# Kernel optimization log

Measured on AMD Instinct MI355X. Metric: run time of the kernel, lower is better.

## Reference

```python
import jax, jax.numpy as jnp
import numpy as np

EPS = 1e-12  # F.normalize default eps

def _l2norm(x, axis):
    n = jnp.sqrt(jnp.sum(x * x, axis=axis, keepdims=True))
    return x / jnp.maximum(n, EPS)

def setup_inputs() -> dict:
    key = jax.random.key(0)
    ks = jax.random.split(key, 12)
    N, D, L, H, R = 65536, 384, 64, 64, 8
    return {
        "enhanced_posts_embeddings": jax.random.normal(ks[0], (N, D), jnp.float32),
        "selected_reasoning_embeddings": jax.random.normal(ks[1], (N, D), jnp.float32),
        "llm_embeddings": jax.random.normal(ks[2], (L, D), jnp.float32),
        "random_num": jax.random.uniform(ks[3], (N, 1), jnp.float32),
        # gate: Linear(2D -> R)
        "gate_w": jax.random.normal(ks[4], (2 * D, R), jnp.float32) * 0.02,
        "gate_b": jnp.zeros((R,), jnp.float32),
        # per-router U: Linear(2D -> H), V: Linear(D -> H)
        "U_w": jax.random.normal(ks[5], (R, 2 * D, H), jnp.float32) * 0.02,
        "U_b": jnp.zeros((R, H), jnp.float32),
        "V_w": jax.random.normal(ks[6], (R, D, H), jnp.float32) * 0.02,
        "V_b": jnp.zeros((R, H), jnp.float32),
    }

def reference(enhanced_posts_embeddings, selected_reasoning_embeddings,
              llm_embeddings, random_num,
              gate_w, gate_b, U_w, U_b, V_w, V_b):
    K = 2
    R = gate_b.shape[0]
    AUX_COEF = 0.05
    TEMP = 1.0

    x = jnp.concatenate([enhanced_posts_embeddings,
                         selected_reasoning_embeddings], axis=-1)  # [N, 2D]
    logits = x @ gate_w + gate_b                                   # [N, R]
    probs = jax.nn.softmax(logits, axis=-1)
    topk_vals, topk_idxs = jax.lax.top_k(logits, K)                # [N, K]
    topk_mask = jax.nn.one_hot(topk_idxs, R, dtype=jnp.float32).sum(axis=1)  # [N, R]

    aux_loss = R * (probs.mean(axis=0) * topk_mask.mean(axis=0)).sum() * AUX_COEF

    # All-router projections (dense over routers), then gather the top-k.
    Ux = _l2norm(jnp.einsum('nd,rdh->nrh', x, U_w) + U_b, axis=-1)            # [N, R, H]
    Vl = _l2norm(jnp.einsum('ld,rdh->rlh', llm_embeddings, V_w) + V_b[:, None, :], axis=-1)  # [R, L, H]
    scores_all = jax.nn.softmax(jnp.einsum('nrh,rlh->nrl', Ux, Vl) / TEMP, axis=-1)  # [N, R, L]

    router_outputs = jnp.take_along_axis(scores_all, topk_idxs[:, :, None], axis=1)  # [N, K, L]
    gate_weights = jax.nn.softmax(topk_vals, axis=-1)[:, :, None]                    # [N, K, 1]
    llm_probs = jnp.sum(router_outputs * gate_weights, axis=1)                       # [N, L]

    scores_cumsum = jnp.cumsum(llm_probs, axis=1)
    selected_index = jnp.argmax((scores_cumsum > random_num).astype(jnp.float32), axis=1)  # [N]
    log_probs = jnp.log(jnp.take_along_axis(llm_probs, selected_index[:, None], axis=1))   # [N, 1]
    return selected_index, log_probs, aux_loss
```

## Files before the change

### kernel.cpp

```cpp
#include <hip/hip_runtime.h>
#include <math.h>

#define AUX_SLOTS 1024
#define CAP 24576

__global__ __launch_bounds__(256) void gate_vl_kernel(
    const float* __restrict__ llm, const float* __restrict__ Vw,
    const float* __restrict__ Vb, float* __restrict__ vl,
    const float* __restrict__ eh, const float* __restrict__ sr,
    const float* __restrict__ gw, const float* __restrict__ gb,
    int* __restrict__ ent, float* __restrict__ ewt,
    float* __restrict__ aux, int* __restrict__ cnt, int N)
{
    __shared__ float red[256];
    __shared__ int lcnt[8], lbase[8], lcur[8];
    __shared__ int   s_r01[32];
    __shared__ float s_w0[32], s_w1[32];
    int tid = threadIdx.x;

    if (blockIdx.x < 512) {
        int b = blockIdx.x;
        int r = b >> 6, l = b & 63;
        int t = tid & 63, q = tid >> 6;
        const float* w  = Vw + ((size_t)r * 384 + q * 96) * 64 + t;
        const float* xr = llm + l * 384 + q * 96;
        float acc = 0.f;
#pragma unroll 4
        for (int d = 0; d < 96; ++d) acc += xr[d] * w[(size_t)d * 64];
        red[tid] = acc;
        __syncthreads();
        if (q == 0) {
            acc = red[t] + red[64 + t] + red[128 + t] + red[192 + t] + Vb[r * 64 + t];
            float ss = acc * acc;
#pragma unroll
            for (int m = 1; m < 64; m <<= 1) ss += __shfl_xor(ss, m);
            float inv = 1.0f / fmaxf(sqrtf(ss), 1e-12f);
            vl[((size_t)r * 64 + t) * 64 + l] = acc * inv;
        }
        return;
    }

    int bx = blockIdx.x - 512;
    if (tid < 8) { lcnt[tid] = 0; lcur[tid] = 0; }
    __syncthreads();
    int wave = tid >> 6, lane = tid & 63;
    int wgid = bx * 4 + wave;
    float gbr[8];
#pragma unroll
    for (int r = 0; r < 8; ++r) gbr[r] = gb[r];
    float aux_acc = 0.f;

    for (int rr = 0; rr < 8; ++rr) {
        int row = wgid * 8 + rr;
        const float4* pa = (const float4*)(eh + (size_t)row * 384);
        const float4* pb = (const float4*)(sr + (size_t)row * 384);
        float4 xv0 = pa[lane];
        const float4* p1 = (lane < 32) ? (pa + 64 + lane) : (pb + (lane - 32));
        float4 xv1 = *p1;
        float4 xv2 = pb[lane + 32];

        float lg[8];
#pragma unroll
        for (int r = 0; r < 8; ++r) lg[r] = 0.f;
        {
            const float* g0 = gw + (size_t)lane * 32;
            const float* g1 = gw + (size_t)(lane + 64) * 32;
            const float* g2 = gw + (size_t)(lane + 128) * 32;
            float xd;
#pragma unroll
            for (int dd = 0; dd < 4; ++dd) {
                xd = (dd == 0) ? xv0.x : (dd == 1) ? xv0.y : (dd == 2) ? xv0.z : xv0.w;
                float4 ga = *(const float4*)(g0 + dd * 8);
                float4 gbv = *(const float4*)(g0 + dd * 8 + 4);
                lg[0] += xd * ga.x;  lg[1] += xd * ga.y;
                lg[2] += xd * ga.z;  lg[3] += xd * ga.w;
                lg[4] += xd * gbv.x; lg[5] += xd * gbv.y;
                lg[6] += xd * gbv.z; lg[7] += xd * gbv.w;
            }
#pragma unroll
            for (int dd = 0; dd < 4; ++dd) {
                xd = (dd == 0) ? xv1.x : (dd == 1) ? xv1.y : (dd == 2) ? xv1.z : xv1.w;
                float4 ga = *(const float4*)(g1 + dd * 8);
                float4 gbv = *(const float4*)(g1 + dd * 8 + 4);
                lg[0] += xd * ga.x;  lg[1] += xd * ga.y;
                lg[2] += xd * ga.z;  lg[3] += xd * ga.w;
                lg[4] += xd * gbv.x; lg[5] += xd * gbv.y;
                lg[6] += xd * gbv.z; lg[7] += xd * gbv.w;
            }
#pragma unroll
            for (int dd = 0; dd < 4; ++dd) {
                xd = (dd == 0) ? xv2.x : (dd == 1) ? xv2.y : (dd == 2) ? xv2.z : xv2.w;
                float4 ga = *(const float4*)(g2 + dd * 8);
                float4 gbv = *(const float4*)(g2 + dd * 8 + 4);
                lg[0] += xd * ga.x;  lg[1] += xd * ga.y;
                lg[2] += xd * ga.z;  lg[3] += xd * ga.w;
                lg[4] += xd * gbv.x; lg[5] += xd * gbv.y;
                lg[6] += xd * gbv.z; lg[7] += xd * gbv.w;
            }
        }
#pragma unroll
        for (int m = 1; m < 64; m <<= 1) {
#pragma unroll
            for (int r = 0; r < 8; ++r) lg[r] += __shfl_xor(lg[r], m);
        }
#pragma unroll
        for (int r = 0; r < 8; ++r) lg[r] += gbr[r];

        float mx = lg[0];
#pragma unroll
        for (int r = 1; r < 8; ++r) mx = fmaxf(mx, lg[r]);
        float e8[8], se = 0.f;
#pragma unroll
        for (int r = 0; r < 8; ++r) { e8[r] = expf(lg[r] - mx); se += e8[r]; }

        int r0 = 0; float v0 = lg[0];
#pragma unroll
        for (int r = 1; r < 8; ++r) if (lg[r] > v0) { v0 = lg[r]; r0 = r; }
        int r1 = (r0 == 0) ? 1 : 0; float v1 = lg[r1];
#pragma unroll
        for (int r = 0; r < 8; ++r) if (r != r1 && r != r0 && lg[r] > v1) { v1 = lg[r]; r1 = r; }
        float z = expf(v1 - v0);
        float w0 = 1.f / (1.f + z), w1 = z / (1.f + z);

        if (lane == 0) {
            s_r01[wave * 8 + rr] = r0 | (r1 << 4);
            s_w0[wave * 8 + rr] = w0;
            s_w1[wave * 8 + rr] = w1;
            atomicAdd(&lcnt[r0], 1);
            atomicAdd(&lcnt[r1], 1);
        }
#pragma unroll
        for (int r2 = 0; r2 < 8; ++r2) {
            if (lane == r2) aux_acc += e8[r2] / se;
            if (lane - 8 == r2) aux_acc += (r2 == r0 || r2 == r1) ? 1.f : 0.f;
        }
    }
    if (lane < 16) atomicAdd(aux + ((size_t)(wgid & (AUX_SLOTS - 1)) * 16) + lane, aux_acc);
    __syncthreads();
    if (tid < 8) lbase[tid] = atomicAdd(&cnt[tid], lcnt[tid]);
    __syncthreads();
    if (tid < 32) {
        int ri = s_r01[tid];
        int row = bx * 32 + tid;
        int r0 = ri & 15, r1 = (ri >> 4) & 15;
        int p0 = lbase[r0] + atomicAdd(&lcur[r0], 1);
        ent[r0 * CAP + p0] = row << 1;       ewt[r0 * CAP + p0] = s_w0[tid];
        int p1 = lbase[r1] + atomicAdd(&lcur[r1], 1);
        ent[r1 * CAP + p1] = (row << 1) | 1; ewt[r1 * CAP + p1] = s_w1[tid];
    }
}

__global__ __launch_bounds__(256, 3) void gemm_kernel(
    const float* __restrict__ eh, const float* __restrict__ sr,
    const float* __restrict__ Uw, const float* __restrict__ Ub,
    const float* __restrict__ vl, const int* __restrict__ ent,
    const float* __restrict__ ewt, const int* __restrict__ cnt,
    float* __restrict__ probs)
{
    int r = blockIdx.y;
    int count = cnt[r]; if (count > CAP) count = CAP;
    int tile = blockIdx.x;
    if (tile * 128 >= count) return;
    int base = r * CAP + tile * 128;

    __shared__ float xs[128 * 32];
    __shared__ float us[32 * 64];
    __shared__ int   sent[128];
    __shared__ float swt[128];

    int tid = threadIdx.x;
    int tx = tid & 7, ty = tid >> 3;
    float4* xs4 = (float4*)xs;
    float4* us4 = (float4*)us;

    if (tid < 128) {
        bool act = (tile * 128 + tid) < count;
        sent[tid] = act ? ent[base + tid] : -1;
        swt[tid]  = act ? ewt[base + tid] : 0.f;
    }
    __syncthreads();

    int rowp[4];
#pragma unroll
    for (int p = 0; p < 4; ++p) {
        int e = sent[ty + 32 * p];
        rowp[p] = (e < 0) ? 0 : (e >> 1);
    }

    float acc[4][8];
#pragma unroll
    for (int i = 0; i < 4; ++i)
#pragma unroll
        for (int j = 0; j < 8; ++j) acc[i][j] = 0.f;

    for (int c = 0; c < 24; ++c) {
        const float* xsrc = (c < 12) ? eh : sr;
        int dd0 = ((c < 12) ? c : c - 12) * 32;
        {
#pragma unroll
            for (int p = 0; p < 4; ++p) {
                int rloc = ty + 32 * p;
                float4 v = ((const float4*)(xsrc + (size_t)rowp[p] * 384 + dd0))[tx];
                xs4[rloc * 8 + (tx ^ ((rloc >> 2) & 7))] = v;
            }
        }
        {
            const float4* pu = (const float4*)(Uw + ((size_t)r * 768 + (size_t)c * 32) * 64);
            us4[tid] = pu[tid];
            us4[tid + 256] = pu[tid + 256];
        }
        __syncthreads();
#pragma unroll
        for (int k4 = 0; k4 < 8; ++k4) {
            float4 a[4];
#pragma unroll
            for (int i = 0; i < 4; ++i)
                a[i] = xs4[(4 * ty + i) * 8 + (k4 ^ (ty & 7))];
#pragma unroll
            for (int j = 0; j < 4; ++j) {
                float4 b0 = us4[(k4 * 4 + j) * 16 + tx * 2];
                float4 b1 = us4[(k4 * 4 + j) * 16 + tx * 2 + 1];
#pragma unroll
                for (int i = 0; i < 4; ++i) {
                    float av = (j == 0) ? a[i].x : (j == 1) ? a[i].y : (j == 2) ? a[i].z : a[i].w;
                    acc[i][0] += av * b0.x; acc[i][1] += av * b0.y;
                    acc[i][2] += av * b0.z; acc[i][3] += av * b0.w;
                    acc[i][4] += av * b1.x; acc[i][5] += av * b1.y;
                    acc[i][6] += av * b1.z; acc[i][7] += av * b1.w;
                }
            }
        }
        __syncthreads();
    }

    float ub[8];
#pragma unroll
    for (int j = 0; j < 8; ++j) ub[j] = Ub[r * 64 + 8 * tx + j];
#pragma unroll
    for (int i = 0; i < 4; ++i) {
        float ss = 0.f;
#pragma unroll
        for (int j = 0; j < 8; ++j) { acc[i][j] += ub[j]; ss += acc[i][j] * acc[i][j]; }
#pragma unroll
        for (int m = 1; m <= 4; m <<= 1) ss += __shfl_xor(ss, m);
        float inv = 1.0f / fmaxf(sqrtf(ss), 1e-12f);
#pragma unroll
        for (int j = 0; j < 8; ++j) acc[i][j] *= inv;
    }

    {
        const float4* pv = (const float4*)(vl + (size_t)r * 4096);
#pragma unroll
        for (int p = 0; p < 4; ++p) {
            int idx = tid + p * 256;
            int h = idx >> 4, l4 = idx & 15;
            xs4[h * 16 + (l4 ^ ((h >> 3) & 7))] = pv[idx];
        }
    }
    __syncthreads();

#pragma unroll
    for (int ih = 0; ih < 4; ih += 2) {
        float sc[2][8];
        for (int lc = 0; lc < 8; ++lc) {
            float part[2][8];
#pragma unroll
            for (int i = 0; i < 2; ++i)
#pragma unroll
                for (int j = 0; j < 8; ++j) part[i][j] = 0.f;
#pragma unroll
            for (int j = 0; j < 8; ++j) {
                int h = 8 * tx + j;
                float4 v0 = xs4[h * 16 + ((2 * lc) ^ tx)];
                float4 v1 = xs4[h * 16 + ((2 * lc + 1) ^ tx)];
#pragma unroll
                for (int i = 0; i < 2; ++i) {
                    float uv = acc[ih + i][j];
                    part[i][0] += uv * v0.x; part[i][1] += uv * v0.y;
                    part[i][2] += uv * v0.z; part[i][3] += uv * v0.w;
                    part[i][4] += uv * v1.x; part[i][5] += uv * v1.y;
                    part[i][6] += uv * v1.z; part[i][7] += uv * v1.w;
                }
            }
#pragma unroll
            for (int m = 1; m <= 4; m <<= 1)
#pragma unroll
                for (int i = 0; i < 2; ++i)
#pragma unroll
                    for (int j = 0; j < 8; ++j) part[i][j] += __shfl_xor(part[i][j], m);
            if (tx == lc) {
#pragma unroll
                for (int i = 0; i < 2; ++i)
#pragma unroll
                    for (int j = 0; j < 8; ++j) sc[i][j] = part[i][j];
            }
        }
#pragma unroll
        for (int i = 0; i < 2; ++i) {
            float mx = sc[i][0];
#pragma unroll
            for (int j = 1; j < 8; ++j) mx = fmaxf(mx, sc[i][j]);
#pragma unroll
            for (int m = 1; m <= 4; m <<= 1) mx = fmaxf(mx, __shfl_xor(mx, m));
            float e[8], ssum = 0.f;
#pragma unroll
            for (int j = 0; j < 8; ++j) { e[j] = expf(sc[i][j] - mx); ssum += e[j]; }
#pragma unroll
            for (int m = 1; m <= 4; m <<= 1) ssum += __shfl_xor(ssum, m);
            int rloc = 4 * ty + ih + i;
            int ei = sent[rloc];
            if (ei >= 0) {
                float w = swt[rloc];
                float4 o0, o1;
                o0.x = (e[0] / ssum) * w; o0.y = (e[1] / ssum) * w;
                o0.z = (e[2] / ssum) * w; o0.w = (e[3] / ssum) * w;
                o1.x = (e[4] / ssum) * w; o1.y = (e[5] / ssum) * w;
                o1.z = (e[6] / ssum) * w; o1.w = (e[7] / ssum) * w;
                size_t bo = (size_t)(ei >> 1) * 128 + (size_t)(ei & 1) * 64 + 8 * tx;
                *(float4*)(probs + bo) = o0;
                *(float4*)(probs + bo + 4) = o1;
            }
        }
    }
}

__global__ __launch_bounds__(256) void combine_kernel(
    const float* __restrict__ probs, const float* __restrict__ rnd,
    const float* __restrict__ aux, float* __restrict__ out, int N)
{
    int w = threadIdx.x >> 6, lane = threadIdx.x & 63;
    int n = blockIdx.x * 4 + w;
    float p = probs[(size_t)n * 128 + lane] + probs[(size_t)n * 128 + 64 + lane];
    float rn = rnd[n];
    float c = 0.f; int sel = 0; bool found = false;
    for (int l = 0; l < 64; ++l) {
        float v = __shfl(p, l);
        c += v;
        if (!found && c > rn) { sel = l; found = true; }
    }
    float pv = __shfl(p, sel);
    if (lane == 0) {
        out[n] = (float)sel;
        out[N + n] = logf(pv);
    }

    if (blockIdx.x == 0) {
        __shared__ float red[256];
        int tid = threadIdx.x;
        int j = tid & 15, s0 = tid >> 4;
        float acc = 0.f;
        for (int s = s0; s < AUX_SLOTS; s += 16) acc += aux[s * 16 + j];
        red[tid] = acc;
        __syncthreads();
        if (tid < 16) {
            float a = 0.f;
            for (int g = 0; g < 16; ++g) a += red[g * 16 + tid];
            red[tid] = a;
        }
        __syncthreads();
        if (tid == 0) {
            float invN = 1.f / (float)N;
            float t = 0.f;
            for (int r2 = 0; r2 < 8; ++r2) t += (red[r2] * invN) * (red[8 + r2] * invN);
            out[2 * N] = 8.0f * 0.05f * t;
        }
    }
}

extern "C" void kernel_launch(void* const* d_in, const int* in_sizes, int n_in,
                              void* d_out, int out_size, void* d_ws, size_t ws_size,
                              hipStream_t stream) {
    const float* eh  = (const float*)d_in[0];
    const float* sr  = (const float*)d_in[1];
    const float* llm = (const float*)d_in[2];
    const float* rnd = (const float*)d_in[3];
    const float* gw  = (const float*)d_in[4];
    const float* gb  = (const float*)d_in[5];
    const float* Uw  = (const float*)d_in[6];
    const float* Ub  = (const float*)d_in[7];
    const float* Vw  = (const float*)d_in[8];
    const float* Vb  = (const float*)d_in[9];
    int N = in_sizes[0] / 384;

    float* vl    = (float*)d_ws;
    float* aux   = vl + 32768;
    int*   cnt   = (int*)(aux + 16384);
    int*   ent   = cnt + 8;
    float* ewt   = (float*)(ent + 8 * CAP);
    float* probs = ewt + 8 * CAP;

    hipMemsetAsync(aux, 0, 16384 * sizeof(float) + 8 * sizeof(int), stream);
    gate_vl_kernel<<<512 + N / 32, 256, 0, stream>>>(llm, Vw, Vb, vl, eh, sr, gw, gb,
                                                     ent, ewt, aux, cnt, N);
    gemm_kernel<<<dim3(CAP / 128, 8), 256, 0, stream>>>(eh, sr, Uw, Ub, vl, ent, ewt,
                                                        cnt, probs);
    combine_kernel<<<N / 4, 256, 0, stream>>>(probs, rnd, aux, (float*)d_out, N);
}
```

Before: 413.9 us.

## Restructure routed GEMM to one row per thread with uniform weight loads

The gemm kernel now uses 128 threads per block, and each thread owns one gathered row with all 64 hidden accumulators in registers. U weights are read straight from global memory at wave-uniform addresses (scalar/broadcast loads) instead of being staged in LDS. The score and softmax stage likewise has each thread compute all 64 logits for its row against a transposed Vl layout, removing the cross-lane shuffle reductions. The cost is high register pressure (64+ accumulators), fewer threads per block, and an occupancy hint of 1, which limits latency hiding.

```diff
diff --git a/kernel.cpp b/kernel.cpp
--- a/kernel.cpp
+++ b/kernel.cpp
@@ -35,7 +35,7 @@
 #pragma unroll
             for (int m = 1; m < 64; m <<= 1) ss += __shfl_xor(ss, m);
             float inv = 1.0f / fmaxf(sqrtf(ss), 1e-12f);
-            vl[((size_t)r * 64 + t) * 64 + l] = acc * inv;
+            vl[(size_t)r * 4096 + l * 64 + t] = acc * inv;
         }
         return;
     }
@@ -150,7 +150,7 @@
     }
 }
 
-__global__ __launch_bounds__(256, 3) void gemm_kernel(
+__global__ __launch_bounds__(128, 1) void gemm_kernel(
     const float* __restrict__ eh, const float* __restrict__ sr,
     const float* __restrict__ Uw, const float* __restrict__ Ub,
     const float* __restrict__ vl, const int* __restrict__ ent,
@@ -163,163 +163,104 @@
     if (tile * 128 >= count) return;
     int base = r * CAP + tile * 128;
 
-    __shared__ float xs[128 * 32];
-    __shared__ float us[32 * 64];
+    __shared__ float lds[8192];
     __shared__ int   sent[128];
     __shared__ float swt[128];
+    float4* xs4 = (float4*)lds;
 
     int tid = threadIdx.x;
-    int tx = tid & 7, ty = tid >> 3;
-    float4* xs4 = (float4*)xs;
-    float4* us4 = (float4*)us;
-
-    if (tid < 128) {
+    {
         bool act = (tile * 128 + tid) < count;
         sent[tid] = act ? ent[base + tid] : -1;
         swt[tid]  = act ? ewt[base + tid] : 0.f;
     }
     __syncthreads();
 
-    int rowp[4];
-#pragma unroll
-    for (int p = 0; p < 4; ++p) {
-        int e = sent[ty + 32 * p];
-        rowp[p] = (e < 0) ? 0 : (e >> 1);
-    }
-
-    float acc[4][8];
-#pragma unroll
-    for (int i = 0; i < 4; ++i)
-#pragma unroll
-        for (int j = 0; j < 8; ++j) acc[i][j] = 0.f;
+    int tx = tid & 7, rg = tid >> 3;
+    int rowst[8];
+#pragma unroll
+    for (int p = 0; p < 8; ++p) {
+        int e = sent[rg + 16 * p];
+        rowst[p] = (e < 0) ? 0 : (e >> 1);
+    }
+    int gmy = (tid ^ (tid >> 3)) & 7;
+
+    float acc[64];
+#pragma unroll
+    for (int h = 0; h < 64; ++h) acc[h] = 0.f;
+
+    const float* ubase = Uw + (size_t)r * 768 * 64;
 
     for (int c = 0; c < 24; ++c) {
         const float* xsrc = (c < 12) ? eh : sr;
         int dd0 = ((c < 12) ? c : c - 12) * 32;
         {
 #pragma unroll
-            for (int p = 0; p < 4; ++p) {
-                int rloc = ty + 32 * p;
-                float4 v = ((const float4*)(xsrc + (size_t)rowp[p] * 384 + dd0))[tx];
-                xs4[rloc * 8 + (tx ^ ((rloc >> 2) & 7))] = v;
-            }
-        }
-        {
-            const float4* pu = (const float4*)(Uw + ((size_t)r * 768 + (size_t)c * 32) * 64);
-            us4[tid] = pu[tid];
-            us4[tid + 256] = pu[tid + 256];
-        }
-        __syncthreads();
-#pragma unroll
-        for (int k4 = 0; k4 < 8; ++k4) {
-            float4 a[4];
-#pragma unroll
-            for (int i = 0; i < 4; ++i)
-                a[i] = xs4[(4 * ty + i) * 8 + (k4 ^ (ty & 7))];
-#pragma unroll
-            for (int j = 0; j < 4; ++j) {
-                float4 b0 = us4[(k4 * 4 + j) * 16 + tx * 2];
-                float4 b1 = us4[(k4 * 4 + j) * 16 + tx * 2 + 1];
-#pragma unroll
-                for (int i = 0; i < 4; ++i) {
-                    float av = (j == 0) ? a[i].x : (j == 1) ? a[i].y : (j == 2) ? a[i].z : a[i].w;
-                    acc[i][0] += av * b0.x; acc[i][1] += av * b0.y;
-                    acc[i][2] += av * b0.z; acc[i][3] += av * b0.w;
-                    acc[i][4] += av * b1.x; acc[i][5] += av * b1.y;
-                    acc[i][6] += av * b1.z; acc[i][7] += av * b1.w;
-                }
-            }
-        }
-        __syncthreads();
-    }
-
-    float ub[8];
-#pragma unroll
-    for (int j = 0; j < 8; ++j) ub[j] = Ub[r * 64 + 8 * tx + j];
-#pragma unroll
-    for (int i = 0; i < 4; ++i) {
+            for (int p = 0; p < 8; ++p) {
+                int rw = rg + 16 * p;
+                float4 v = ((const float4*)(xsrc + (size_t)rowst[p] * 384 + dd0))[tx];
+                xs4[rw * 8 + (tx ^ ((rw ^ (rw >> 3)) & 7))] = v;
+            }
+        }
+        __syncthreads();
+        const float* up0 = ubase + (size_t)c * 32 * 64;
+        for (int k8 = 0; k8 < 4; ++k8) {
+            float4 xa = xs4[tid * 8 + ((2 * k8) ^ gmy)];
+            float4 xb = xs4[tid * 8 + ((2 * k8 + 1) ^ gmy)];
+            const float* up = up0 + k8 * 512;
+#pragma unroll
+            for (int kk = 0; kk < 8; ++kk) {
+                float xk = (kk == 0) ? xa.x : (kk == 1) ? xa.y : (kk == 2) ? xa.z :
+                           (kk == 3) ? xa.w : (kk == 4) ? xb.x : (kk == 5) ? xb.y :
+                           (kk == 6) ? xb.z : xb.w;
+#pragma unroll
+                for (int h = 0; h < 64; ++h)
+                    acc[h] = fmaf(up[kk * 64 + h], xk, acc[h]);
+            }
+        }
+        __syncthreads();
+    }
+
+    {
+        const float* ubp = Ub + r * 64;
         float ss = 0.f;
 #pragma unroll
-        for (int j = 0; j < 8; ++j) { acc[i][j] += ub[j]; ss += acc[i][j] * acc[i][j]; }
-#pragma unroll
-        for (int m = 1; m <= 4; m <<= 1) ss += __shfl_xor(ss, m);
+        for (int h = 0; h < 64; ++h) { acc[h] += ubp[h]; ss += acc[h] * acc[h]; }
         float inv = 1.0f / fmaxf(sqrtf(ss), 1e-12f);
 #pragma unroll
-        for (int j = 0; j < 8; ++j) acc[i][j] *= inv;
-    }
-
-    {
-        const float4* pv = (const float4*)(vl + (size_t)r * 4096);
-#pragma unroll
-        for (int p = 0; p < 4; ++p) {
-            int idx = tid + p * 256;
-            int h = idx >> 4, l4 = idx & 15;
-            xs4[h * 16 + (l4 ^ ((h >> 3) & 7))] = pv[idx];
-        }
-    }
-    __syncthreads();
-
-#pragma unroll
-    for (int ih = 0; ih < 4; ih += 2) {
-        float sc[2][8];
-        for (int lc = 0; lc < 8; ++lc) {
-            float part[2][8];
-#pragma unroll
-            for (int i = 0; i < 2; ++i)
-#pragma unroll
-                for (int j = 0; j < 8; ++j) part[i][j] = 0.f;
-#pragma unroll
-            for (int j = 0; j < 8; ++j) {
-                int h = 8 * tx + j;
-                float4 v0 = xs4[h * 16 + ((2 * lc) ^ tx)];
-                float4 v1 = xs4[h * 16 + ((2 * lc + 1) ^ tx)];
-#pragma unroll
-                for (int i = 0; i < 2; ++i) {
-                    float uv = acc[ih + i][j];
-                    part[i][0] += uv * v0.x; part[i][1] += uv * v0.y;
-                    part[i][2] += uv * v0.z; part[i][3] += uv * v0.w;
-                    part[i][4] += uv * v1.x; part[i][5] += uv * v1.y;
-                    part[i][6] += uv * v1.z; part[i][7] += uv * v1.w;
-                }
-            }
-#pragma unroll
-            for (int m = 1; m <= 4; m <<= 1)
-#pragma unroll
-                for (int i = 0; i < 2; ++i)
-#pragma unroll
-                    for (int j = 0; j < 8; ++j) part[i][j] += __shfl_xor(part[i][j], m);
-            if (tx == lc) {
-#pragma unroll
-                for (int i = 0; i < 2; ++i)
-#pragma unroll
-                    for (int j = 0; j < 8; ++j) sc[i][j] = part[i][j];
-            }
-        }
-#pragma unroll
-        for (int i = 0; i < 2; ++i) {
-            float mx = sc[i][0];
-#pragma unroll
-            for (int j = 1; j < 8; ++j) mx = fmaxf(mx, sc[i][j]);
-#pragma unroll
-            for (int m = 1; m <= 4; m <<= 1) mx = fmaxf(mx, __shfl_xor(mx, m));
-            float e[8], ssum = 0.f;
-#pragma unroll
-            for (int j = 0; j < 8; ++j) { e[j] = expf(sc[i][j] - mx); ssum += e[j]; }
-#pragma unroll
-            for (int m = 1; m <= 4; m <<= 1) ssum += __shfl_xor(ssum, m);
-            int rloc = 4 * ty + ih + i;
-            int ei = sent[rloc];
-            if (ei >= 0) {
-                float w = swt[rloc];
-                float4 o0, o1;
-                o0.x = (e[0] / ssum) * w; o0.y = (e[1] / ssum) * w;
-                o0.z = (e[2] / ssum) * w; o0.w = (e[3] / ssum) * w;
-                o1.x = (e[4] / ssum) * w; o1.y = (e[5] / ssum) * w;
-                o1.z = (e[6] / ssum) * w; o1.w = (e[7] / ssum) * w;
-                size_t bo = (size_t)(ei >> 1) * 128 + (size_t)(ei & 1) * 64 + 8 * tx;
-                *(float4*)(probs + bo) = o0;
-                *(float4*)(probs + bo + 4) = o1;
-            }
+        for (int h = 0; h < 64; ++h) acc[h] *= inv;
+    }
+
+    const float* vp = vl + (size_t)r * 4096;
+    int sw = tid & 63;
+    float mx = -3.4e38f;
+    for (int l = 0; l < 64; ++l) {
+        const float* vpl = vp + l * 64;
+        float sl = 0.f;
+#pragma unroll
+        for (int h = 0; h < 64; ++h) sl = fmaf(vpl[h], acc[h], sl);
+        lds[tid * 64 + (l ^ sw)] = sl;
+        mx = fmaxf(mx, sl);
+    }
+    float ssum = 0.f;
+    for (int l = 0; l < 64; ++l) {
+        int a = tid * 64 + (l ^ sw);
+        float e = expf(lds[a] - mx);
+        ssum += e;
+        lds[a] = e;
+    }
+    int ei = sent[tid];
+    if (ei >= 0) {
+        float wsc = swt[tid] / ssum;
+        size_t bo = (size_t)(ei >> 1) * 128 + (size_t)(ei & 1) * 64;
+#pragma unroll
+        for (int l4 = 0; l4 < 16; ++l4) {
+            float4 o;
+            o.x = lds[tid * 64 + ((4 * l4 + 0) ^ sw)] * wsc;
+            o.y = lds[tid * 64 + ((4 * l4 + 1) ^ sw)] * wsc;
+            o.z = lds[tid * 64 + ((4 * l4 + 2) ^ sw)] * wsc;
+            o.w = lds[tid * 64 + ((4 * l4 + 3) ^ sw)] * wsc;
+            *(float4*)(probs + bo + 4 * l4) = o;
         }
     }
 }
@@ -392,7 +333,7 @@
     hipMemsetAsync(aux, 0, 16384 * sizeof(float) + 8 * sizeof(int), stream);
     gate_vl_kernel<<<512 + N / 32, 256, 0, stream>>>(llm, Vw, Vb, vl, eh, sr, gw, gb,
                                                      ent, ewt, aux, cnt, N);
-    gemm_kernel<<<dim3(CAP / 128, 8), 256, 0, stream>>>(eh, sr, Uw, Ub, vl, ent, ewt,
+    gemm_kernel<<<dim3(CAP / 128, 8), 128, 0, stream>>>(eh, sr, Uw, Ub, vl, ent, ewt,
                                                         cnt, probs);
     combine_kernel<<<N / 4, 256, 0, stream>>>(probs, rnd, aux, (float*)d_out, N);
 }
```

New measurement: 642.3 us. 55.2% more time.
